# Kernel tuning notes

Hardware: AMD Instinct MI355X
Metric: run time of the kernel (lower is better)

The kernel has to match this reference:

```python
import jax, jax.numpy as jnp
import numpy as np

N, T = 8192, 8192
RB, CB = 32, 32
HID = 100


def setup_inputs() -> dict:
    key = jax.random.key(0)
    ks = jax.random.split(key, 10)
    X = jax.random.normal(ks[0], (N, T), dtype=jnp.float32)
    # sorted segment ids emulate the multinomial block partition (row/col cumsum boundaries)
    row_ids = jnp.sort(jax.random.randint(ks[1], (N,), 0, RB)).astype(jnp.int32)
    col_ids = jnp.sort(jax.random.randint(ks[2], (T,), 0, CB)).astype(jnp.int32)
    d_io = RB * CB
    s1 = 1.0 / np.sqrt(d_io)
    s2 = 1.0 / np.sqrt(HID)
    W1 = jax.random.uniform(ks[3], (d_io, HID), jnp.float32, -s1, s1)
    b1 = jnp.zeros((HID,), jnp.float32)
    W2 = jax.random.uniform(ks[4], (HID, HID), jnp.float32, -s2, s2)
    b2 = jnp.zeros((HID,), jnp.float32)
    W3 = jax.random.uniform(ks[5], (HID, d_io), jnp.float32, -s2, s2)
    b3 = jnp.zeros((d_io,), jnp.float32)
    return {"X": X, "row_ids": row_ids, "col_ids": col_ids,
            "W1": W1, "b1": b1, "W2": W2, "b2": b2, "W3": W3, "b3": b3}


def _block_mean(X, row_ids, col_ids):
    # single-pass segmented reduce replacing the nested Python loop over blocks
    row_sum = jax.ops.segment_sum(X, row_ids, num_segments=RB)            # [RB, T]
    blk_sum = jax.ops.segment_sum(row_sum.T, col_ids, num_segments=CB).T  # [RB, CB]
    rcnt = jnp.bincount(row_ids, length=RB).astype(jnp.float32)
    ccnt = jnp.bincount(col_ids, length=CB).astype(jnp.float32)
    cnt = jnp.maximum(rcnt[:, None] * ccnt[None, :], 1.0)
    return blk_sum / cnt


def _mar_mlp(x_small, W1, b1, W2, b2, W3, b3):
    # 3-layer relu MLP propensity generator (MAR_missingness), sigmoid output
    h = x_small.reshape(-1)
    h = jax.nn.relu(h @ W1 + b1)
    h = jax.nn.relu(h @ W2 + b2)
    return jax.nn.sigmoid(h @ W3 + b3).reshape(RB, CB)


def reference(X, row_ids, col_ids, W1, b1, W2, b2, W3, b3):
    X_small = _block_mean(X, row_ids, col_ids)
    propensity = _mar_mlp(X_small, W1, b1, W2, b2, W3, b3)
    row_cumsum = jnp.concatenate([jnp.zeros((1,), jnp.int32),
                                  jnp.cumsum(jnp.bincount(row_ids, length=RB)).astype(jnp.int32)])
    col_cumsum = jnp.concatenate([jnp.zeros((1,), jnp.int32),
                                  jnp.cumsum(jnp.bincount(col_ids, length=CB)).astype(jnp.int32)])
    return propensity, row_cumsum, col_cumsum
```

## Files before the change

kernel.cpp:

```cpp
#include <hip/hip_runtime.h>
#include <math.h>

#define N 8192
#define T 8192
#define RB 32
#define CB 32
#define HID 100
#define DIO (RB*CB)

#define ROWS_PER_BLOCK 64
#define COLS_PER_BLOCK 1024
#define NBLK ((T/COLS_PER_BLOCK)*(N/ROWS_PER_BLOCK))
#define K1BLOCKS 32
#define KCHUNK (DIO/K1BLOCKS)

__global__ void k_bounds(const int* __restrict__ row_ids, const int* __restrict__ col_ids,
                         int* __restrict__ rc, int* __restrict__ cc) {
    int tid = blockIdx.x * blockDim.x + threadIdx.x;
    int stride = gridDim.x * blockDim.x;
    for (int i = tid; i < N; i += stride) {
        int a = row_ids[i];
        int b = (i + 1 < N) ? row_ids[i + 1] : RB;
        for (int k = a + 1; k <= b; ++k) rc[k] = i + 1;
        if (i == 0) { for (int k = 0; k <= a; ++k) rc[k] = 0; }
    }
    for (int i = tid; i < T; i += stride) {
        int a = col_ids[i];
        int b = (i + 1 < T) ? col_ids[i + 1] : CB;
        for (int k = a + 1; k <= b; ++k) cc[k] = i + 1;
        if (i == 0) { for (int k = 0; k <= a; ++k) cc[k] = 0; }
    }
}

__global__ __launch_bounds__(256) void k_blocksum(const float* __restrict__ X,
        const int* __restrict__ row_ids, const int* __restrict__ col_ids,
        const int* __restrict__ rc, float* __restrict__ blk) {
    __shared__ float lblk[DIO];
    __shared__ int src[RB + 1];
    for (int i = threadIdx.x; i < DIO; i += 256) lblk[i] = 0.f;
    if (threadIdx.x < RB + 1) src[threadIdx.x] = rc[threadIdx.x];
    __syncthreads();

    const int colTile  = blockIdx.x & 7;
    const int rowChunk = blockIdx.x >> 3;
    const int c0 = colTile * COLS_PER_BLOCK + threadIdx.x * 4;

    const int cs0 = col_ids[c0 + 0];
    const int cs1 = col_ids[c0 + 1];
    const int cs2 = col_ids[c0 + 2];
    const int cs3 = col_ids[c0 + 3];

    const float4* __restrict__ X4 = (const float4*)X;
    const int i0   = rowChunk * ROWS_PER_BLOCK;
    const int iend = i0 + ROWS_PER_BLOCK;
    const size_t cidx = (size_t)(c0 >> 2);

    const int sFirst = row_ids[i0];
    const int sLast  = row_ids[iend - 1];

    if (sFirst == sLast) {
        float a0 = 0.f, a1 = 0.f, a2 = 0.f, a3 = 0.f;
        #pragma unroll 8
        for (int i = i0; i < iend; ++i) {
            float4 x = X4[(size_t)i * (T / 4) + cidx];
            a0 += x.x; a1 += x.y; a2 += x.z; a3 += x.w;
        }
        atomicAdd(&lblk[sFirst * CB + cs0], a0);
        atomicAdd(&lblk[sFirst * CB + cs1], a1);
        atomicAdd(&lblk[sFirst * CB + cs2], a2);
        atomicAdd(&lblk[sFirst * CB + cs3], a3);
    } else {
        int i = i0;
        int s = sFirst;
        while (i < iend) {
            int hi = min(src[s + 1], iend);
            float a0 = 0.f, a1 = 0.f, a2 = 0.f, a3 = 0.f;
            for (; i < hi; ++i) {
                float4 x = X4[(size_t)i * (T / 4) + cidx];
                a0 += x.x; a1 += x.y; a2 += x.z; a3 += x.w;
            }
            atomicAdd(&lblk[s * CB + cs0], a0);
            atomicAdd(&lblk[s * CB + cs1], a1);
            atomicAdd(&lblk[s * CB + cs2], a2);
            atomicAdd(&lblk[s * CB + cs3], a3);
            ++s;
        }
    }

    __syncthreads();
    for (int i = threadIdx.x; i < DIO; i += 256) {
        float v = lblk[i];
        if (v != 0.f) atomicAdd(&blk[i], v);
    }
}

__global__ __launch_bounds__(128) void k_mlp1(const float* __restrict__ blk,
        const int* __restrict__ rc, const int* __restrict__ cc,
        const float* __restrict__ W1, float* __restrict__ part1) {
    __shared__ float xs[KCHUNK];
    const int b = blockIdx.x, t = threadIdx.x;
    const int k0 = b * KCHUNK;
    if (t < KCHUNK) {
        int k = k0 + t;
        int r = k >> 5, c = k & 31;
        float cnt = fmaxf((float)(rc[r + 1] - rc[r]) * (float)(cc[c + 1] - cc[c]), 1.0f);
        xs[t] = blk[k] / cnt;
    }
    __syncthreads();
    if (t < HID) {
        float s = 0.f;
        #pragma unroll 8
        for (int kk = 0; kk < KCHUNK; ++kk)
            s += xs[kk] * W1[(size_t)(k0 + kk) * HID + t];
        part1[b * HID + t] = s;
    }
}

__global__ __launch_bounds__(128) void k_mlp2(const float* __restrict__ part1,
        const float* __restrict__ b1, const float* __restrict__ W2,
        const float* __restrict__ b2, const int* __restrict__ rc,
        const int* __restrict__ cc, float* __restrict__ h2out,
        float* __restrict__ out) {
    __shared__ float h1[HID];
    const int t = threadIdx.x;
    if (t < HID) {
        float s = b1[t];
        #pragma unroll 8
        for (int b = 0; b < K1BLOCKS; ++b) s += part1[b * HID + t];
        h1[t] = fmaxf(s, 0.f);
    }
    __syncthreads();
    if (t < HID) {
        float s = b2[t];
        #pragma unroll 4
        for (int k = 0; k < HID; ++k) s += h1[k] * W2[k * HID + t];
        h2out[t] = fmaxf(s, 0.f);
    }
    if (t < RB + 1) out[DIO + t] = (float)rc[t];
    if (t < CB + 1) out[DIO + RB + 1 + t] = (float)cc[t];
}

__global__ __launch_bounds__(128) void k_mlp3(const float* __restrict__ h2,
        const float* __restrict__ W3, const float* __restrict__ b3,
        float* __restrict__ out) {
    __shared__ float h[HID];
    const int t = threadIdx.x;
    if (t < HID) h[t] = h2[t];
    __syncthreads();
    const int o = blockIdx.x * 128 + t;
    float s = b3[o];
    #pragma unroll 4
    for (int k = 0; k < HID; ++k) s += h[k] * W3[k * DIO + o];
    out[o] = 1.f / (1.f + expf(-s));
}

extern "C" void kernel_launch(void* const* d_in, const int* in_sizes, int n_in,
                              void* d_out, int out_size, void* d_ws, size_t ws_size,
                              hipStream_t stream) {
    const float* X       = (const float*)d_in[0];
    const int*   row_ids = (const int*)  d_in[1];
    const int*   col_ids = (const int*)  d_in[2];
    const float* W1      = (const float*)d_in[3];
    const float* b1      = (const float*)d_in[4];
    const float* W2      = (const float*)d_in[5];
    const float* b2      = (const float*)d_in[6];
    const float* W3      = (const float*)d_in[7];
    const float* b3      = (const float*)d_in[8];
    float* out = (float*)d_out;

    float* blk   = (float*)d_ws;
    float* part1 = blk + DIO;
    float* h2    = part1 + K1BLOCKS * HID;
    int*   rc    = (int*)(h2 + HID);
    int*   cc    = rc + (RB + 1);

    hipMemsetAsync(blk, 0, DIO * sizeof(float), stream);

    k_bounds<<<16, 256, 0, stream>>>(row_ids, col_ids, rc, cc);
    k_blocksum<<<NBLK, 256, 0, stream>>>(X, row_ids, col_ids, rc, blk);
    k_mlp1<<<K1BLOCKS, 128, 0, stream>>>(blk, rc, cc, W1, part1);
    k_mlp2<<<1, 128, 0, stream>>>(part1, b1, W2, b2, rc, cc, h2, out);
    k_mlp3<<<DIO / 128, 128, 0, stream>>>(h2, W3, b3, out);
}
```

Baseline: 424.2 us.

## Restructure block-sum to full-row tiles with wavefront segmented reduction into global atomics

The block-sum kernel now gives each workgroup 8 full rows, and each thread keeps 8 float4 accumulators across the whole row width. It replaces the shared-memory block accumulator with a wavefront shuffle segmented reduction keyed by column segment, then does direct global atomics. The memset is folded into the bounds kernel to drop one launch. This cuts shared memory and syncthreads overhead and raises per-thread memory-level parallelism, but it issues many more global atomics, because each of 1024 workgroups flushes per segment.

```diff
diff --git a/kernel.cpp b/kernel.cpp
--- a/kernel.cpp
+++ b/kernel.cpp
@@ -8,16 +8,16 @@
 #define HID 100
 #define DIO (RB*CB)
 
-#define ROWS_PER_BLOCK 64
-#define COLS_PER_BLOCK 1024
-#define NBLK ((T/COLS_PER_BLOCK)*(N/ROWS_PER_BLOCK))
+#define RPB 8
+#define BS_BLOCKS (N / RPB)
 #define K1BLOCKS 32
 #define KCHUNK (DIO/K1BLOCKS)
 
 __global__ void k_bounds(const int* __restrict__ row_ids, const int* __restrict__ col_ids,
-                         int* __restrict__ rc, int* __restrict__ cc) {
+                         int* __restrict__ rc, int* __restrict__ cc, float* __restrict__ blk) {
     int tid = blockIdx.x * blockDim.x + threadIdx.x;
     int stride = gridDim.x * blockDim.x;
+    for (int i = tid; i < DIO; i += stride) blk[i] = 0.f;
     for (int i = tid; i < N; i += stride) {
         int a = row_ids[i];
         int b = (i + 1 < N) ? row_ids[i + 1] : RB;
@@ -32,65 +32,75 @@
     }
 }
 
+__device__ __forceinline__ void flush_seg(float4* acc, const int4* __restrict__ col_ids4,
+                                          int t, int rs, float* __restrict__ blk) {
+    const int lane = t & 63;
+    #pragma unroll
+    for (int j = 0; j < 8; ++j) {
+        int4 cs = col_ids4[t + 256 * j];
+        int key = cs.x;
+        float v;
+        if (cs.w == key) {
+            v = acc[j].x + acc[j].y + acc[j].z + acc[j].w;
+        } else {
+            v = acc[j].x;
+            if (cs.y == key) v += acc[j].y; else atomicAdd(&blk[rs * CB + cs.y], acc[j].y);
+            if (cs.z == key) v += acc[j].z; else atomicAdd(&blk[rs * CB + cs.z], acc[j].z);
+            if (cs.w == key) v += acc[j].w; else atomicAdd(&blk[rs * CB + cs.w], acc[j].w);
+        }
+        #pragma unroll
+        for (int d = 1; d < 64; d <<= 1) {
+            float vv = __shfl_down(v, d, 64);
+            int   kk = __shfl_down(key, d, 64);
+            if (lane + d < 64 && kk == key) v += vv;
+        }
+        int kprev = __shfl_up(key, 1, 64);
+        if (lane == 0 || kprev != key)
+            atomicAdd(&blk[rs * CB + key], v);
+        acc[j] = make_float4(0.f, 0.f, 0.f, 0.f);
+    }
+}
+
 __global__ __launch_bounds__(256) void k_blocksum(const float* __restrict__ X,
         const int* __restrict__ row_ids, const int* __restrict__ col_ids,
-        const int* __restrict__ rc, float* __restrict__ blk) {
-    __shared__ float lblk[DIO];
-    __shared__ int src[RB + 1];
-    for (int i = threadIdx.x; i < DIO; i += 256) lblk[i] = 0.f;
-    if (threadIdx.x < RB + 1) src[threadIdx.x] = rc[threadIdx.x];
-    __syncthreads();
+        float* __restrict__ blk) {
+    const int t = threadIdx.x;
+    const int b = blockIdx.x;
+    const int r0 = b * RPB;
+    const float4* __restrict__ X4 = (const float4*)X;
+    const int4*   __restrict__ C4 = (const int4*)col_ids;
 
-    const int colTile  = blockIdx.x & 7;
-    const int rowChunk = blockIdx.x >> 3;
-    const int c0 = colTile * COLS_PER_BLOCK + threadIdx.x * 4;
+    float4 acc[8];
+    #pragma unroll
+    for (int j = 0; j < 8; ++j) acc[j] = make_float4(0.f, 0.f, 0.f, 0.f);
 
-    const int cs0 = col_ids[c0 + 0];
-    const int cs1 = col_ids[c0 + 1];
-    const int cs2 = col_ids[c0 + 2];
-    const int cs3 = col_ids[c0 + 3];
+    const int4* rid4 = (const int4*)(row_ids + r0);
+    int4 ra = rid4[0], rb = rid4[1];
 
-    const float4* __restrict__ X4 = (const float4*)X;
-    const int i0   = rowChunk * ROWS_PER_BLOCK;
-    const int iend = i0 + ROWS_PER_BLOCK;
-    const size_t cidx = (size_t)(c0 >> 2);
-
-    const int sFirst = row_ids[i0];
-    const int sLast  = row_ids[iend - 1];
-
-    if (sFirst == sLast) {
-        float a0 = 0.f, a1 = 0.f, a2 = 0.f, a3 = 0.f;
-        #pragma unroll 8
-        for (int i = i0; i < iend; ++i) {
-            float4 x = X4[(size_t)i * (T / 4) + cidx];
-            a0 += x.x; a1 += x.y; a2 += x.z; a3 += x.w;
+    if (ra.x == rb.w) {
+        #pragma unroll
+        for (int r = 0; r < RPB; ++r) {
+            const float4* __restrict__ row = X4 + (size_t)(r0 + r) * (T / 4);
+            #pragma unroll
+            for (int j = 0; j < 8; ++j) {
+                float4 x = row[t + 256 * j];
+                acc[j].x += x.x; acc[j].y += x.y; acc[j].z += x.z; acc[j].w += x.w;
+            }
         }
-        atomicAdd(&lblk[sFirst * CB + cs0], a0);
-        atomicAdd(&lblk[sFirst * CB + cs1], a1);
-        atomicAdd(&lblk[sFirst * CB + cs2], a2);
-        atomicAdd(&lblk[sFirst * CB + cs3], a3);
+        flush_seg(acc, C4, t, ra.x, blk);
     } else {
-        int i = i0;
-        int s = sFirst;
-        while (i < iend) {
-            int hi = min(src[s + 1], iend);
-            float a0 = 0.f, a1 = 0.f, a2 = 0.f, a3 = 0.f;
-            for (; i < hi; ++i) {
-                float4 x = X4[(size_t)i * (T / 4) + cidx];
-                a0 += x.x; a1 += x.y; a2 += x.z; a3 += x.w;
+        int rseg[RPB] = {ra.x, ra.y, ra.z, ra.w, rb.x, rb.y, rb.z, rb.w};
+        int cur = rseg[0];
+        for (int r = 0; r < RPB; ++r) {
+            if (rseg[r] != cur) { flush_seg(acc, C4, t, cur, blk); cur = rseg[r]; }
+            const float4* __restrict__ row = X4 + (size_t)(r0 + r) * (T / 4);
+            #pragma unroll
+            for (int j = 0; j < 8; ++j) {
+                float4 x = row[t + 256 * j];
+                acc[j].x += x.x; acc[j].y += x.y; acc[j].z += x.z; acc[j].w += x.w;
             }
-            atomicAdd(&lblk[s * CB + cs0], a0);
-            atomicAdd(&lblk[s * CB + cs1], a1);
-            atomicAdd(&lblk[s * CB + cs2], a2);
-            atomicAdd(&lblk[s * CB + cs3], a3);
-            ++s;
         }
-    }
-
-    __syncthreads();
-    for (int i = threadIdx.x; i < DIO; i += 256) {
-        float v = lblk[i];
-        if (v != 0.f) atomicAdd(&blk[i], v);
+        flush_seg(acc, C4, t, cur, blk);
     }
 }
 
@@ -174,10 +184,8 @@
     int*   rc    = (int*)(h2 + HID);
     int*   cc    = rc + (RB + 1);
 
-    hipMemsetAsync(blk, 0, DIO * sizeof(float), stream);
-
-    k_bounds<<<16, 256, 0, stream>>>(row_ids, col_ids, rc, cc);
-    k_blocksum<<<NBLK, 256, 0, stream>>>(X, row_ids, col_ids, rc, blk);
+    k_bounds<<<16, 256, 0, stream>>>(row_ids, col_ids, rc, cc, blk);
+    k_blocksum<<<BS_BLOCKS, 256, 0, stream>>>(X, row_ids, col_ids, blk);
     k_mlp1<<<K1BLOCKS, 128, 0, stream>>>(blk, rc, cc, W1, part1);
     k_mlp2<<<1, 128, 0, stream>>>(part1, b1, W2, b2, rc, cc, h2, out);
     k_mlp3<<<DIO / 128, 128, 0, stream>>>(h2, W3, b3, out);
```

Measured after the change: 425.3 us (median of 2 runs). Within noise of the previous version (+0.3%).
